# Kernel optimization log

Hardware: AMD Instinct MI355X
Metric: run time of the kernel (lower is better)

The kernel has to match this reference:

```python
import jax, jax.numpy as jnp
import numpy as np

H = 4  # num_heads


def transformer_conv(x, src, dst, wq, bq, wk, bk, wv, bv, ws, bs):
    # PyG TransformerConv, concat=False, root_weight=True, eval mode (no dropout).
    N = x.shape[0]
    C = wq.shape[1] // H  # per-head channels
    q = (x @ wq + bq).reshape(N, H, C)
    k = (x @ wk + bk).reshape(N, H, C)
    v = (x @ wv + bv).reshape(N, H, C)
    # per-edge attention logits: query at dst, key at src
    logits = (q[dst] * k[src]).sum(-1) / jnp.sqrt(jnp.asarray(C, x.dtype))  # [E,H]
    # scatter-softmax over incoming edges of each destination node
    m = jax.lax.stop_gradient(jax.ops.segment_max(logits, dst, num_segments=N))
    m = jnp.where(jnp.isfinite(m), m, jnp.zeros_like(m))
    e = jnp.exp(logits - m[dst])
    denom = jax.ops.segment_sum(e, dst, num_segments=N)
    alpha = e / (denom[dst] + 1e-16)  # [E,H]
    out = jax.ops.segment_sum(alpha[:, :, None] * v[src], dst, num_segments=N)  # [N,H,C]
    return out.mean(axis=1) + x @ ws + bs  # head-average + skip


def setup_inputs() -> dict:
    key = jax.random.key(0)
    ks = jax.random.split(key, 16)
    N, E, D, HID, OUT = 50000, 800000, 128, 32, 40
    s = 0.05
    inp = {
        "x": jax.random.normal(ks[0], (N, D), jnp.float32),
        "edge_index": jax.random.randint(ks[1], (2, E), 0, N, jnp.int64),
        "wq1": jax.random.normal(ks[2], (D, H * HID), jnp.float32) * s,
        "bq1": jnp.zeros((H * HID,), jnp.float32),
        "wk1": jax.random.normal(ks[3], (D, H * HID), jnp.float32) * s,
        "bk1": jnp.zeros((H * HID,), jnp.float32),
        "wv1": jax.random.normal(ks[4], (D, H * HID), jnp.float32) * s,
        "bv1": jnp.zeros((H * HID,), jnp.float32),
        "ws1": jax.random.normal(ks[5], (D, HID), jnp.float32) * s,
        "bs1": jnp.zeros((HID,), jnp.float32),
        "wq2": jax.random.normal(ks[6], (HID, H * HID), jnp.float32) * s,
        "bq2": jnp.zeros((H * HID,), jnp.float32),
        "wk2": jax.random.normal(ks[7], (HID, H * HID), jnp.float32) * s,
        "bk2": jnp.zeros((H * HID,), jnp.float32),
        "wv2": jax.random.normal(ks[8], (HID, H * HID), jnp.float32) * s,
        "bv2": jnp.zeros((H * HID,), jnp.float32),
        "ws2": jax.random.normal(ks[9], (HID, HID), jnp.float32) * s,
        "bs2": jnp.zeros((HID,), jnp.float32),
        "wc": jax.random.normal(ks[10], (HID, OUT), jnp.float32) * s,
        "bc": jnp.zeros((OUT,), jnp.float32),
    }
    return inp


def reference(x, edge_index, wq1, bq1, wk1, bk1, wv1, bv1, ws1, bs1,
              wq2, bq2, wk2, bk2, wv2, bv2, ws2, bs2, wc, bc):
    src, dst = edge_index[0], edge_index[1]
    h = jax.nn.relu(transformer_conv(x, src, dst, wq1, bq1, wk1, bk1, wv1, bv1, ws1, bs1))
    h = jax.nn.relu(transformer_conv(h, src, dst, wq2, bq2, wk2, bk2, wv2, bv2, ws2, bs2))
    return h @ wc + bc
```

## Files before the change

kernel.cpp:

```cpp
#include <hip/hip_runtime.h>
#include <hip/hip_bf16.h>

typedef __attribute__((ext_vector_type(8))) short short8;
typedef __attribute__((ext_vector_type(4))) float floatx4;
typedef __attribute__((ext_vector_type(4))) unsigned short ushort4v;

__device__ inline unsigned short f2bf(float x) {
    unsigned int u = __float_as_uint(x);
    u += 0x7FFFu + ((u >> 16) & 1u);
    return (unsigned short)(u >> 16);
}
__device__ inline float bf2f(unsigned short h) {
    return __uint_as_float(((unsigned int)h) << 16);
}
__device__ inline float blo(unsigned int u) { return __uint_as_float(u << 16); }
__device__ inline float bhi(unsigned int u) { return __uint_as_float(u & 0xFFFF0000u); }

#if defined(__has_builtin)
#if __has_builtin(__builtin_amdgcn_exp2f)
#define EXP2F(x) __builtin_amdgcn_exp2f(x)
#else
#define EXP2F(x) exp2f(x)
#endif
#if __has_builtin(__builtin_amdgcn_update_dpp)
#define HAVE_DPP 1
#endif
#else
#define EXP2F(x) exp2f(x)
#endif

#ifdef HAVE_DPP
template <int CTRL>
__device__ __forceinline__ float dppadd(float x) {
    int s = __builtin_amdgcn_update_dpp(0, __float_as_int(x), CTRL, 0xf, 0xf, true);
    return x + __int_as_float(s);
}
__device__ __forceinline__ float red8(float x) {
    x = dppadd<0xB1>(x);
    x = dppadd<0x4E>(x);
    x = dppadd<0x141>(x);
    return x;
}
__device__ __forceinline__ float xor8add(float x) {
    return dppadd<0x128>(x);
}
#else
__device__ __forceinline__ float red8(float x) {
    x += __shfl_xor(x, 1); x += __shfl_xor(x, 2); x += __shfl_xor(x, 4);
    return x;
}
__device__ __forceinline__ float xor8add(float x) { return x + __shfl_xor(x, 8); }
#endif

template <bool B> struct BC { static constexpr bool value = B; };

__global__ __launch_bounds__(256) void hist_kernel(
    const int* __restrict__ dst, int* __restrict__ deg, int E)
{
    int e = blockIdx.x * blockDim.x + threadIdx.x;
    if (e < E) atomicAdd(&deg[dst[e]], 1);
}

__global__ __launch_bounds__(256) void scan_part(
    const int* __restrict__ deg, int* __restrict__ bsum, int N)
{
    __shared__ int ws[4];
    const int base = blockIdx.x * 1024;
    const int tid = threadIdx.x, lane = tid & 63, w = tid >> 6;
    int s = 0;
#pragma unroll
    for (int j = 0; j < 4; j++) {
        int i = base + j * 256 + tid;
        if (i < N) s += deg[i];
    }
#pragma unroll
    for (int off = 1; off < 64; off <<= 1) s += __shfl_xor(s, off, 64);
    if (lane == 0) ws[w] = s;
    __syncthreads();
    if (tid == 0) bsum[blockIdx.x] = ws[0] + ws[1] + ws[2] + ws[3];
}

__global__ __launch_bounds__(64) void scan_tops(
    const int* __restrict__ bsum, int* __restrict__ boff,
    int* __restrict__ rowptr, int nb, int N)
{
    int lane = threadIdx.x;
    int v = (lane < nb) ? bsum[lane] : 0;
    int inc = v;
#pragma unroll
    for (int off = 1; off < 64; off <<= 1) {
        int t = __shfl_up(inc, off, 64);
        if (lane >= off) inc += t;
    }
    if (lane < nb) boff[lane] = inc - v;
    if (lane == 63) rowptr[N] = inc;
}

__global__ __launch_bounds__(256) void scan_final(
    const int* __restrict__ deg, const int* __restrict__ boff,
    int* __restrict__ rowptr, int* __restrict__ cursor, int N)
{
    __shared__ int woff[4];
    const int base = blockIdx.x * 1024;
    const int tid = threadIdx.x, lane = tid & 63, w = tid >> 6;
    const int i0 = base + tid * 4;
    int v0 = (i0     < N) ? deg[i0]     : 0;
    int v1 = (i0 + 1 < N) ? deg[i0 + 1] : 0;
    int v2 = (i0 + 2 < N) ? deg[i0 + 2] : 0;
    int v3 = (i0 + 3 < N) ? deg[i0 + 3] : 0;
    int ts = v0 + v1 + v2 + v3;
    int inc = ts;
#pragma unroll
    for (int off = 1; off < 64; off <<= 1) {
        int t = __shfl_up(inc, off, 64);
        if (lane >= off) inc += t;
    }
    if (lane == 63) woff[w] = inc;
    __syncthreads();
    int wpre = 0;
    if (w > 0) wpre += woff[0];
    if (w > 1) wpre += woff[1];
    if (w > 2) wpre += woff[2];
    int exc = boff[blockIdx.x] + wpre + inc - ts;
    int p0 = exc, p1 = exc + v0, p2 = p1 + v1, p3 = p2 + v2;
    if (i0     < N) { rowptr[i0]     = p0; cursor[i0]     = p0; }
    if (i0 + 1 < N) { rowptr[i0 + 1] = p1; cursor[i0 + 1] = p1; }
    if (i0 + 2 < N) { rowptr[i0 + 2] = p2; cursor[i0 + 2] = p2; }
    if (i0 + 3 < N) { rowptr[i0 + 3] = p3; cursor[i0 + 3] = p3; }
}

__global__ __launch_bounds__(256) void fill_kernel(
    const int* __restrict__ src, const int* __restrict__ dst,
    int* __restrict__ cursor, int* __restrict__ perm, int E)
{
    int e = blockIdx.x * blockDim.x + threadIdx.x;
    if (e >= E) return;
    int pos = atomicAdd(&cursor[dst[e]], 1);
    perm[pos] = src[e];
}

__global__ __launch_bounds__(128) void wprep_all(
    const float* __restrict__ wq1, const float* __restrict__ bq1,
    const float* __restrict__ wk1, const float* __restrict__ bk1,
    const float* __restrict__ wv1, const float* __restrict__ bv1,
    const float* __restrict__ ws1, const float* __restrict__ bs1,
    const float* __restrict__ wq2, const float* __restrict__ bq2,
    const float* __restrict__ wk2, const float* __restrict__ bk2,
    const float* __restrict__ wv2, const float* __restrict__ bv2,
    const float* __restrict__ ws2, const float* __restrict__ bs2,
    unsigned short* __restrict__ wt1h, unsigned short* __restrict__ wt1l,
    float* __restrict__ bias1,
    unsigned short* __restrict__ wt2h, unsigned short* __restrict__ wt2l,
    float* __restrict__ bias2)
{
    const int layer = (blockIdx.x >= 416) ? 1 : 0;
    const int c = blockIdx.x - layer * 416;
    const int t = threadIdx.x;
    const int L = layer ? 32 : 128;
    if (t >= L) return;
    const float* w; const float* b; int cc, ncols;
    if (c < 384) {
        int m = c >> 7; cc = c & 127; ncols = 128;
        if (layer == 0) {
            w = (m == 0) ? wq1 : ((m == 1) ? wk1 : wv1);
            b = (m == 0) ? bq1 : ((m == 1) ? bk1 : bv1);
        } else {
            w = (m == 0) ? wq2 : ((m == 1) ? wk2 : wv2);
            b = (m == 0) ? bq2 : ((m == 1) ? bk2 : bv2);
        }
    } else {
        cc = c - 384; ncols = 32;
        w = layer ? ws2 : ws1; b = layer ? bs2 : bs1;
    }
    unsigned short* wh = layer ? wt2h : wt1h;
    unsigned short* wl = layer ? wt2l : wt1l;
    float* bias = layer ? bias2 : bias1;
    const float QSCL = 0.17677669529663687f * 1.4426950408889634f;
    const float f = (c < 128) ? QSCL : 1.0f;
    float val = w[t * ncols + cc] * f;
    unsigned short h = f2bf(val);
    wh[c * L + t] = h;
    wl[c * L + t] = f2bf(val - bf2f(h));
    if (t == 0) bias[c] = b[cc] * f;
}

template <int L>
__global__ __launch_bounds__(256) void proj_mfma(
    const float* __restrict__ xin,
    const unsigned short* __restrict__ wt_hi,
    const unsigned short* __restrict__ wt_lo,
    const float* __restrict__ bias,
    float* __restrict__ q, unsigned short* __restrict__ kvp,
    float* __restrict__ skip, int N)
{
    constexpr int LP = L + 8;
    constexpr int KS = L / 32;
    constexpr int SI = (32 * (L / 4)) / 256;
    __shared__ unsigned short xh[2][32 * LP];
    __shared__ unsigned short xl[2][32 * LP];
    __shared__ float scr[4][32 * 36];
    const int tid = threadIdx.x, lane = tid & 63, w = tid >> 6;
    const int li = lane & 15, quad = lane >> 4;
    const int slot = __builtin_amdgcn_readfirstlane(blockIdx.y * 4 + w);
    const bool hasT = slot < 13;

    int t0 = 24, t1 = 25;
    if (slot < 4)       { t0 = slot * 2; t1 = t0 + 1; }
    else if (slot < 12) { t0 = 4 + slot; t1 = 12 + slot; }

    short8 Ah[2][KS], Al[2][KS];
    float bias_r[2][4];
    if (hasT) {
#pragma unroll
        for (int ti = 0; ti < 2; ti++) {
            int tt = ti ? t1 : t0;
#pragma unroll
            for (int ks = 0; ks < KS; ks++) {
                long off = (long)(tt * 16 + li) * L + ks * 32 + quad * 8;
                Ah[ti][ks] = *(const short8*)(wt_hi + off);
                Al[ti][ks] = *(const short8*)(wt_lo + off);
            }
#pragma unroll
            for (int r = 0; r < 4; r++)
                bias_r[ti][r] = bias[tt * 16 + quad * 4 + r];
        }
    }

    const int nb0 = blockIdx.x * 256;
    float* myscr = scr[w];
    unsigned int* su = (unsigned int*)myscr;

    float4 xv[SI];
    auto issue_loads = [&](int c) {
#pragma unroll
        for (int s = 0; s < SI; s++) {
            int f = s * 256 + tid;
            int row = f / (L / 4), c4 = (f - row * (L / 4)) * 4;
            int n = nb0 + c * 32 + row;
            xv[s] = (n < N) ? *(const float4*)(xin + (long)n * L + c4)
                            : make_float4(0.f, 0.f, 0.f, 0.f);
        }
    };
    auto cvt_store = [&](int buf) {
#pragma unroll
        for (int s = 0; s < SI; s++) {
            int f = s * 256 + tid;
            int row = f / (L / 4), c4 = (f - row * (L / 4)) * 4;
            unsigned short h0 = f2bf(xv[s].x), h1 = f2bf(xv[s].y),
                           h2 = f2bf(xv[s].z), h3 = f2bf(xv[s].w);
            ushort4v hs = {h0, h1, h2, h3};
            ushort4v ls = {f2bf(xv[s].x - bf2f(h0)), f2bf(xv[s].y - bf2f(h1)),
                           f2bf(xv[s].z - bf2f(h2)), f2bf(xv[s].w - bf2f(h3))};
            *(ushort4v*)(xh[buf] + row * LP + c4) = hs;
            *(ushort4v*)(xl[buf] + row * LP + c4) = ls;
        }
    };

    issue_loads(0);
    cvt_store(0);
    __syncthreads();

    for (int c = 0; c < 8; c++) {
        if (c < 7) issue_loads(c + 1);
        const int n0c = nb0 + c * 32;
        if (hasT) {
            const int buf = c & 1;
#pragma unroll
            for (int half = 0; half < 2; half++) {
                short8 Bh[KS], Bl[KS];
#pragma unroll
                for (int ks = 0; ks < KS; ks++) {
                    int off = (half * 16 + li) * LP + ks * 32 + quad * 8;
                    Bh[ks] = *(const short8*)(xh[buf] + off);
                    Bl[ks] = *(const short8*)(xl[buf] + off);
                }
                floatx4 accv[2];
#pragma unroll
                for (int ti = 0; ti < 2; ti++) {
                    floatx4 acc = {0.f, 0.f, 0.f, 0.f};
#pragma unroll
                    for (int ks = 0; ks < KS; ks++) {
                        acc = __builtin_amdgcn_mfma_f32_16x16x32_bf16(Ah[ti][ks], Bh[ks], acc, 0, 0, 0);
                        acc = __builtin_amdgcn_mfma_f32_16x16x32_bf16(Ah[ti][ks], Bl[ks], acc, 0, 0, 0);
                        acc = __builtin_amdgcn_mfma_f32_16x16x32_bf16(Al[ti][ks], Bh[ks], acc, 0, 0, 0);
                    }
#pragma unroll
                    for (int r = 0; r < 4; r++) acc[r] += bias_r[ti][r];
                    accv[ti] = acc;
                }
                const int row = half * 16 + li;
                if (slot < 4 || slot == 12) {
                    *(floatx4*)(myscr + row * 36 + quad * 4)      = accv[0];
                    *(floatx4*)(myscr + row * 36 + 16 + quad * 4) = accv[1];
                } else {
                    unsigned int k01 = (unsigned int)f2bf(accv[0][0]) | ((unsigned int)f2bf(accv[0][1]) << 16);
                    unsigned int k23 = (unsigned int)f2bf(accv[0][2]) | ((unsigned int)f2bf(accv[0][3]) << 16);
                    unsigned int v01 = (unsigned int)f2bf(accv[1][0]) | ((unsigned int)f2bf(accv[1][1]) << 16);
                    unsigned int v23 = (unsigned int)f2bf(accv[1][2]) | ((unsigned int)f2bf(accv[1][3]) << 16);
                    uint4 pk = make_uint4(k01, v01, k23, v23);
                    *(uint4*)(su + row * 20 + quad * 4) = pk;
                }
            }
            if (slot < 4) {
#pragma unroll
                for (int it = 0; it < 4; it++) {
                    int idx = it * 64 + lane;
                    int nl = idx >> 3, seg = idx & 7;
                    int node = n0c + nl;
                    if (node < N) {
                        floatx4 vv = *(floatx4*)(myscr + nl * 36 + seg * 4);
                        *(floatx4*)(q + (long)node * 128 + slot * 32 + seg * 4) = vv;
                    }
                }
            } else if (slot == 12) {
#pragma unroll
                for (int it = 0; it < 4; it++) {
                    int idx = it * 64 + lane;
                    int nl = idx >> 3, seg = idx & 7;
                    int node = n0c + nl;
                    if (node < N) {
                        floatx4 vv = *(floatx4*)(myscr + nl * 36 + seg * 4);
                        *(floatx4*)(skip + (long)node * 32 + seg * 4) = vv;
                    }
                }
            } else {
                const int i = slot - 4;
#pragma unroll
                for (int it = 0; it < 2; it++) {
                    int idx = it * 64 + lane;
                    int nl = idx >> 2, part = idx & 3;
                    int node = n0c + nl;
                    if (node < N) {
                        uint4 vv = *(uint4*)(su + nl * 20 + part * 4);
                        *(uint4*)((unsigned int*)(kvp + (long)node * 256) + i * 16 + part * 4) = vv;
                    }
                }
            }
        }
        __syncthreads();
        if (c < 7) cvt_store((c + 1) & 1);
        __syncthreads();
    }
}

template <bool FUSE_CLS>
__global__ __launch_bounds__(256) void attn_kernel(
    const float* __restrict__ q, const unsigned short* __restrict__ kvp,
    const int* __restrict__ rowptr, const int* __restrict__ perm,
    const float* __restrict__ skip, float* __restrict__ h,
    const float* __restrict__ wc, const float* __restrict__ bc,
    float* __restrict__ out, int N, int E)
{
    __shared__ float hrow[4][32];
    const int tid = threadIdx.x;
    const int wid = (blockIdx.x * 256 + tid) >> 6;
    const int wv = (tid >> 6) & 3;
    const int lane = tid & 63;
    if (wid >= N) return;
    const int d = __builtin_amdgcn_readfirstlane(wid);
    const int eh = lane >> 5;
    const int sl = lane & 31;
    const int hh = sl >> 3;
    const int g  = sl & 7;
    const unsigned dby = (unsigned)(hh * 64 + g * 8) * 2u;
    const char* __restrict__ kvb = (const char*)kvp;
    const float4 q4 = *(const float4*)(q + (long)d * 128 + hh * 32 + g * 4);

    const int beg = rowptr[d], end = rowptr[d + 1];
    const int n = end - beg;
    const int na = (n + 1) >> 1;
    const int nmin = n - na;
    const int my_off = beg + (eh ? na : 0);
    const int my_cnt = eh ? nmin : na;
    const int* __restrict__ pp = perm + my_off;

    float den = 0.f;
    float o0 = 0.f, o1 = 0.f, o2 = 0.f, o3 = 0.f;

    auto kvld = [&](int s) -> uint4 {
        return *(const uint4*)(kvb + ((((unsigned)s) << 9) + dby));
    };

    uint4 A0, A1, A2, A3, B0, B1, B2, B3, C0, C1, C2, C3;
    int PA0, PA1, PA2, PA3, PB0, PB1, PB2, PB3, PC0, PC1, PC2, PC3;
    {
        int i0 = pp[0], i1 = pp[1], i2  = pp[2],  i3  = pp[3];
        int i4 = pp[4], i5 = pp[5], i6  = pp[6],  i7  = pp[7];
        int i8 = pp[8], i9 = pp[9], i10 = pp[10], i11 = pp[11];
        PA0 = pp[12]; PA1 = pp[13]; PA2 = pp[14]; PA3 = pp[15];
        PB0 = pp[16]; PB1 = pp[17]; PB2 = pp[18]; PB3 = pp[19];
        PC0 = pp[20]; PC1 = pp[21]; PC2 = pp[22]; PC3 = pp[23];
        A0 = kvld(i0); A1 = kvld(i1); A2 = kvld(i2);  A3 = kvld(i3);
        B0 = kvld(i4); B1 = kvld(i5); B2 = kvld(i6);  B3 = kvld(i7);
        C0 = kvld(i8); C1 = kvld(i9); C2 = kvld(i10); C3 = kvld(i11);
    }

    auto grp = [&](const uint4& G0, const uint4& G1, const uint4& G2,
                   const uint4& G3, int jb, auto mc) {
        constexpr bool MASKED = decltype(mc)::value;
        float p0 = q4.x * blo(G0.x) + q4.y * bhi(G0.x) + q4.z * blo(G0.z) + q4.w * bhi(G0.z);
        float p1 = q4.x * blo(G1.x) + q4.y * bhi(G1.x) + q4.z * blo(G1.z) + q4.w * bhi(G1.z);
        float p2 = q4.x * blo(G2.x) + q4.y * bhi(G2.x) + q4.z * blo(G2.z) + q4.w * bhi(G2.z);
        float p3 = q4.x * blo(G3.x) + q4.y * bhi(G3.x) + q4.z * blo(G3.z) + q4.w * bhi(G3.z);
        p0 = red8(p0); p1 = red8(p1); p2 = red8(p2); p3 = red8(p3);
        p0 = fminf(p0, 60.f); p1 = fminf(p1, 60.f);
        p2 = fminf(p2, 60.f); p3 = fminf(p3, 60.f);
        if (MASKED) {
            p0 = (jb + 0 < my_cnt) ? p0 : -INFINITY;
            p1 = (jb + 1 < my_cnt) ? p1 : -INFINITY;
            p2 = (jb + 2 < my_cnt) ? p2 : -INFINITY;
            p3 = (jb + 3 < my_cnt) ? p3 : -INFINITY;
        }
        const float w0 = EXP2F(p0), w1 = EXP2F(p1);
        const float w2 = EXP2F(p2), w3 = EXP2F(p3);
        den += (w0 + w1) + (w2 + w3);
        o0 += w0 * blo(G0.y) + w1 * blo(G1.y) + w2 * blo(G2.y) + w3 * blo(G3.y);
        o1 += w0 * bhi(G0.y) + w1 * bhi(G1.y) + w2 * bhi(G2.y) + w3 * bhi(G3.y);
        o2 += w0 * blo(G0.w) + w1 * blo(G1.w) + w2 * blo(G2.w) + w3 * blo(G3.w);
        o3 += w0 * bhi(G0.w) + w1 * bhi(G1.w) + w2 * bhi(G2.w) + w3 * bhi(G3.w);
    };

    int j = 0;
    for (; j + 12 <= nmin; j += 12) {
        grp(A0, A1, A2, A3, j, BC<false>{});
        A0 = kvld(PA0); A1 = kvld(PA1); A2 = kvld(PA2); A3 = kvld(PA3);
        PA0 = pp[j + 24]; PA1 = pp[j + 25]; PA2 = pp[j + 26]; PA3 = pp[j + 27];
        grp(B0, B1, B2, B3, j + 4, BC<false>{});
        B0 = kvld(PB0); B1 = kvld(PB1); B2 = kvld(PB2); B3 = kvld(PB3);
        PB0 = pp[j + 28]; PB1 = pp[j + 29]; PB2 = pp[j + 30]; PB3 = pp[j + 31];
        grp(C0, C1, C2, C3, j + 8, BC<false>{});
        C0 = kvld(PC0); C1 = kvld(PC1); C2 = kvld(PC2); C3 = kvld(PC3);
        PC0 = pp[j + 32]; PC1 = pp[j + 33]; PC2 = pp[j + 34]; PC3 = pp[j + 35];
    }
    if (j < na) {
        grp(A0, A1, A2, A3, j, BC<true>{});
        if (j + 4 < na) grp(B0, B1, B2, B3, j + 4, BC<true>{});
        if (j + 8 < na) grp(C0, C1, C2, C3, j + 8, BC<true>{});
    }

    den += __shfl_xor(den, 32);
    o0 += __shfl_xor(o0, 32);
    o1 += __shfl_xor(o1, 32);
    o2 += __shfl_xor(o2, 32);
    o3 += __shfl_xor(o3, 32);

    const float inv = 1.f / (den + 1e-16f);
    o0 *= inv; o1 *= inv; o2 *= inv; o3 *= inv;
    o0 = xor8add(o0); o1 = xor8add(o1);
    o2 = xor8add(o2); o3 = xor8add(o3);
    o0 += __shfl_xor(o0, 16); o1 += __shfl_xor(o1, 16);
    o2 += __shfl_xor(o2, 16); o3 += __shfl_xor(o3, 16);

    if (lane < 8) {
        float4 sk = *(const float4*)(skip + (long)d * 32 + g * 4);
        float r0 = 0.25f * o0 + sk.x;
        float r1 = 0.25f * o1 + sk.y;
        float r2 = 0.25f * o2 + sk.z;
        float r3 = 0.25f * o3 + sk.w;
        r0 = r0 > 0.f ? r0 : 0.f;
        r1 = r1 > 0.f ? r1 : 0.f;
        r2 = r2 > 0.f ? r2 : 0.f;
        r3 = r3 > 0.f ? r3 : 0.f;
        if (FUSE_CLS) {
            *(float4*)&hrow[wv][g * 4] = make_float4(r0, r1, r2, r3);
        } else {
            *(float4*)(h + (long)d * 32 + g * 4) = make_float4(r0, r1, r2, r3);
        }
    }
    if (FUSE_CLS) {
        __builtin_amdgcn_wave_barrier();
        if (lane < 40) {
            float acc = bc[lane];
#pragma unroll
            for (int l = 0; l < 32; ++l)
                acc = fmaf(hrow[wv][l], wc[l * 40 + lane], acc);
            out[(long)d * 40 + lane] = acc;
        }
    }
}

extern "C" void kernel_launch(void* const* d_in, const int* in_sizes, int n_in,
                              void* d_out, int out_size, void* d_ws, size_t ws_size,
                              hipStream_t stream)
{
    const float* x   = (const float*)d_in[0];
    const int* ei    = (const int*)d_in[1];
    const float* wq1 = (const float*)d_in[2];  const float* bq1 = (const float*)d_in[3];
    const float* wk1 = (const float*)d_in[4];  const float* bk1 = (const float*)d_in[5];
    const float* wv1 = (const float*)d_in[6];  const float* bv1 = (const float*)d_in[7];
    const float* ws1 = (const float*)d_in[8];  const float* bs1 = (const float*)d_in[9];
    const float* wq2 = (const float*)d_in[10]; const float* bq2 = (const float*)d_in[11];
    const float* wk2 = (const float*)d_in[12]; const float* bk2 = (const float*)d_in[13];
    const float* wv2 = (const float*)d_in[14]; const float* bv2 = (const float*)d_in[15];
    const float* ws2 = (const float*)d_in[16]; const float* bs2 = (const float*)d_in[17];
    const float* wc  = (const float*)d_in[18]; const float* bc  = (const float*)d_in[19];

    const int N = in_sizes[0] / 128;
    const int E = in_sizes[1] / 2;
    const int* src = ei;
    const int* dst = ei + E;

    char* p = (char*)d_ws;
    auto take = [&](size_t bytes) { char* r = p; p += (bytes + 255) & ~(size_t)255; return r; };
    float* q             = (float*)take((size_t)N * 128 * 4);
    unsigned short* kvp  = (unsigned short*)take((size_t)N * 256 * 2);
    float* skip          = (float*)take((size_t)N * 32 * 4);
    float* h1            = (float*)take((size_t)N * 32 * 4);
    unsigned short* wt1h = (unsigned short*)take(416 * 128 * 2);
    unsigned short* wt1l = (unsigned short*)take(416 * 128 * 2);
    unsigned short* wt2h = (unsigned short*)take(416 * 32 * 2);
    unsigned short* wt2l = (unsigned short*)take(416 * 32 * 2);
    float* bias1         = (float*)take(416 * 4);
    float* bias2         = (float*)take(416 * 4);
    int* deg             = (int*)take((size_t)N * 4);
    int* rowptr          = (int*)take((size_t)(N + 1) * 4);
    int* cursor          = (int*)take((size_t)N * 4);
    int* perm            = (int*)take((size_t)(E + 48) * 4);
    int* bsum            = (int*)take(64 * 4);
    int* boff            = (int*)take(64 * 4);

    const dim3 projGrid((N + 255) / 256, 4);
    const int eGrid    = (E + 255) / 256;
    const int attnGrid = (N + 3) / 4;
    const int nb       = (N + 1023) / 1024;

    wprep_all<<<832, 128, 0, stream>>>(wq1, bq1, wk1, bk1, wv1, bv1, ws1, bs1,
                                       wq2, bq2, wk2, bk2, wv2, bv2, ws2, bs2,
                                       wt1h, wt1l, bias1, wt2h, wt2l, bias2);
    hipMemsetAsync(deg, 0, (size_t)N * 4, stream);
    hipMemsetAsync(perm + E, 0, 48 * 4, stream);
    hist_kernel<<<eGrid, 256, 0, stream>>>(dst, deg, E);
    scan_part<<<nb, 256, 0, stream>>>(deg, bsum, N);
    scan_tops<<<1, 64, 0, stream>>>(bsum, boff, rowptr, nb, N);
    scan_final<<<nb, 256, 0, stream>>>(deg, boff, rowptr, cursor, N);
    fill_kernel<<<eGrid, 256, 0, stream>>>(src, dst, cursor, perm, E);

    proj_mfma<128><<<projGrid, 256, 0, stream>>>(x, wt1h, wt1l, bias1, q, kvp, skip, N);
    attn_kernel<false><<<attnGrid, 256, 0, stream>>>(q, kvp, rowptr, perm, skip, h1,
                                                     wc, bc, (float*)d_out, N, E);

    proj_mfma<32><<<projGrid, 256, 0, stream>>>(h1, wt2h, wt2l, bias2, q, kvp, skip, N);
    attn_kernel<true><<<attnGrid, 256, 0, stream>>>(q, kvp, rowptr, perm, skip, h1,
                                                    wc, bc, (float*)d_out, N, E);
}
```

Baseline: 365.1 us.

## Fuse CSR build kernels into weight prep and projection, load x directly into registers

Merges the weight-prep kernel with the degree histogram, and merges the CSR fill pass into the layer-1 projection launch as extra blocks. The perm padding clear moves into scan_tops, dropping a memset. The projection kernel now runs 512-thread blocks with 8 waves and no LDS staging of x: each wave loads its own x rows from global memory into registers, splits them into bf16 hi/lo, and uses wave barriers instead of block barriers. This removes several launches and the block-wide syncs, at the cost of each wave reloading the same x tile, so global/L2 traffic goes up, and fill atomics now compete with the projection work.

```diff
diff --git a/kernel.cpp b/kernel.cpp
--- a/kernel.cpp
+++ b/kernel.cpp
@@ -3,7 +3,6 @@
 
 typedef __attribute__((ext_vector_type(8))) short short8;
 typedef __attribute__((ext_vector_type(4))) float floatx4;
-typedef __attribute__((ext_vector_type(4))) unsigned short ushort4v;
 
 __device__ inline unsigned short f2bf(float x) {
     unsigned int u = __float_as_uint(x);
@@ -54,11 +53,56 @@
 
 template <bool B> struct BC { static constexpr bool value = B; };
 
-__global__ __launch_bounds__(256) void hist_kernel(
+__global__ __launch_bounds__(256) void wprep_hist(
+    const float* __restrict__ wq1, const float* __restrict__ bq1,
+    const float* __restrict__ wk1, const float* __restrict__ bk1,
+    const float* __restrict__ wv1, const float* __restrict__ bv1,
+    const float* __restrict__ ws1, const float* __restrict__ bs1,
+    const float* __restrict__ wq2, const float* __restrict__ bq2,
+    const float* __restrict__ wk2, const float* __restrict__ bk2,
+    const float* __restrict__ wv2, const float* __restrict__ bv2,
+    const float* __restrict__ ws2, const float* __restrict__ bs2,
+    unsigned short* __restrict__ wt1h, unsigned short* __restrict__ wt1l,
+    float* __restrict__ bias1,
+    unsigned short* __restrict__ wt2h, unsigned short* __restrict__ wt2l,
+    float* __restrict__ bias2,
     const int* __restrict__ dst, int* __restrict__ deg, int E)
 {
-    int e = blockIdx.x * blockDim.x + threadIdx.x;
-    if (e < E) atomicAdd(&deg[dst[e]], 1);
+    const int bx = blockIdx.x;
+    const int t = threadIdx.x;
+    if (bx >= 832) {
+        int e = (bx - 832) * 256 + t;
+        if (e < E) atomicAdd(&deg[dst[e]], 1);
+        return;
+    }
+    const int layer = (bx >= 416) ? 1 : 0;
+    const int c = bx - layer * 416;
+    const int L = layer ? 32 : 128;
+    if (t >= L) return;
+    const float* w; const float* b; int cc, ncols;
+    if (c < 384) {
+        int m = c >> 7; cc = c & 127; ncols = 128;
+        if (layer == 0) {
+            w = (m == 0) ? wq1 : ((m == 1) ? wk1 : wv1);
+            b = (m == 0) ? bq1 : ((m == 1) ? bk1 : bv1);
+        } else {
+            w = (m == 0) ? wq2 : ((m == 1) ? wk2 : wv2);
+            b = (m == 0) ? bq2 : ((m == 1) ? bk2 : bv2);
+        }
+    } else {
+        cc = c - 384; ncols = 32;
+        w = layer ? ws2 : ws1; b = layer ? bs2 : bs1;
+    }
+    unsigned short* wh = layer ? wt2h : wt1h;
+    unsigned short* wl = layer ? wt2l : wt1l;
+    float* bias = layer ? bias2 : bias1;
+    const float QSCL = 0.17677669529663687f * 1.4426950408889634f;
+    const float f = (c < 128) ? QSCL : 1.0f;
+    float val = w[t * ncols + cc] * f;
+    unsigned short h = f2bf(val);
+    wh[c * L + t] = h;
+    wl[c * L + t] = f2bf(val - bf2f(h));
+    if (t == 0) bias[c] = b[cc] * f;
 }
 
 __global__ __launch_bounds__(256) void scan_part(
@@ -82,9 +126,11 @@
 
 __global__ __launch_bounds__(64) void scan_tops(
     const int* __restrict__ bsum, int* __restrict__ boff,
-    int* __restrict__ rowptr, int nb, int N)
+    int* __restrict__ rowptr, int nb, int N,
+    int* __restrict__ perm, int E)
 {
     int lane = threadIdx.x;
+    if (lane < 48) perm[E + lane] = 0;
     int v = (lane < nb) ? bsum[lane] : 0;
     int inc = v;
 #pragma unroll
@@ -129,217 +175,150 @@
     if (i0 + 3 < N) { rowptr[i0 + 3] = p3; cursor[i0 + 3] = p3; }
 }
 
-__global__ __launch_bounds__(256) void fill_kernel(
-    const int* __restrict__ src, const int* __restrict__ dst,
-    int* __restrict__ cursor, int* __restrict__ perm, int E)
-{
-    int e = blockIdx.x * blockDim.x + threadIdx.x;
-    if (e >= E) return;
-    int pos = atomicAdd(&cursor[dst[e]], 1);
-    perm[pos] = src[e];
-}
-
-__global__ __launch_bounds__(128) void wprep_all(
-    const float* __restrict__ wq1, const float* __restrict__ bq1,
-    const float* __restrict__ wk1, const float* __restrict__ bk1,
-    const float* __restrict__ wv1, const float* __restrict__ bv1,
-    const float* __restrict__ ws1, const float* __restrict__ bs1,
-    const float* __restrict__ wq2, const float* __restrict__ bq2,
-    const float* __restrict__ wk2, const float* __restrict__ bk2,
-    const float* __restrict__ wv2, const float* __restrict__ bv2,
-    const float* __restrict__ ws2, const float* __restrict__ bs2,
-    unsigned short* __restrict__ wt1h, unsigned short* __restrict__ wt1l,
-    float* __restrict__ bias1,
-    unsigned short* __restrict__ wt2h, unsigned short* __restrict__ wt2l,
-    float* __restrict__ bias2)
-{
-    const int layer = (blockIdx.x >= 416) ? 1 : 0;
-    const int c = blockIdx.x - layer * 416;
-    const int t = threadIdx.x;
-    const int L = layer ? 32 : 128;
-    if (t >= L) return;
-    const float* w; const float* b; int cc, ncols;
-    if (c < 384) {
-        int m = c >> 7; cc = c & 127; ncols = 128;
-        if (layer == 0) {
-            w = (m == 0) ? wq1 : ((m == 1) ? wk1 : wv1);
-            b = (m == 0) ? bq1 : ((m == 1) ? bk1 : bv1);
-        } else {
-            w = (m == 0) ? wq2 : ((m == 1) ? wk2 : wv2);
-            b = (m == 0) ? bq2 : ((m == 1) ? bk2 : bv2);
-        }
-    } else {
-        cc = c - 384; ncols = 32;
-        w = layer ? ws2 : ws1; b = layer ? bs2 : bs1;
-    }
-    unsigned short* wh = layer ? wt2h : wt1h;
-    unsigned short* wl = layer ? wt2l : wt1l;
-    float* bias = layer ? bias2 : bias1;
-    const float QSCL = 0.17677669529663687f * 1.4426950408889634f;
-    const float f = (c < 128) ? QSCL : 1.0f;
-    float val = w[t * ncols + cc] * f;
-    unsigned short h = f2bf(val);
-    wh[c * L + t] = h;
-    wl[c * L + t] = f2bf(val - bf2f(h));
-    if (t == 0) bias[c] = b[cc] * f;
-}
-
 template <int L>
-__global__ __launch_bounds__(256) void proj_mfma(
+__global__ __launch_bounds__(512) void proj_reg(
     const float* __restrict__ xin,
     const unsigned short* __restrict__ wt_hi,
     const unsigned short* __restrict__ wt_lo,
     const float* __restrict__ bias,
     float* __restrict__ q, unsigned short* __restrict__ kvp,
-    float* __restrict__ skip, int N)
-{
-    constexpr int LP = L + 8;
+    float* __restrict__ skip, int N, int projNB,
+    const int* __restrict__ src, const int* __restrict__ dst,
+    int* __restrict__ cursor, int* __restrict__ perm, int E)
+{
     constexpr int KS = L / 32;
-    constexpr int SI = (32 * (L / 4)) / 256;
-    __shared__ unsigned short xh[2][32 * LP];
-    __shared__ unsigned short xl[2][32 * LP];
-    __shared__ float scr[4][32 * 36];
-    const int tid = threadIdx.x, lane = tid & 63, w = tid >> 6;
+    __shared__ float scr[8][32 * 36];
+
+    const int bx = blockIdx.x;
+    const int tid = threadIdx.x;
+    if (bx >= projNB * 2) {
+        int e = (bx - projNB * 2) * 512 + tid;
+        if (e < E) {
+            int pos = atomicAdd(&cursor[dst[e]], 1);
+            perm[pos] = src[e];
+        }
+        return;
+    }
+
+    const int lane = tid & 63, w = tid >> 6;
     const int li = lane & 15, quad = lane >> 4;
-    const int slot = __builtin_amdgcn_readfirstlane(blockIdx.y * 4 + w);
-    const bool hasT = slot < 13;
-
-    int t0 = 24, t1 = 25;
+    const int slot = __builtin_amdgcn_readfirstlane((bx & 1) * 8 + w);
+    if (slot >= 13) return;
+
+    int t0, t1;
     if (slot < 4)       { t0 = slot * 2; t1 = t0 + 1; }
     else if (slot < 12) { t0 = 4 + slot; t1 = 12 + slot; }
+    else                { t0 = 24; t1 = 25; }
 
     short8 Ah[2][KS], Al[2][KS];
     float bias_r[2][4];
-    if (hasT) {
-#pragma unroll
-        for (int ti = 0; ti < 2; ti++) {
-            int tt = ti ? t1 : t0;
-#pragma unroll
-            for (int ks = 0; ks < KS; ks++) {
-                long off = (long)(tt * 16 + li) * L + ks * 32 + quad * 8;
-                Ah[ti][ks] = *(const short8*)(wt_hi + off);
-                Al[ti][ks] = *(const short8*)(wt_lo + off);
-            }
-#pragma unroll
-            for (int r = 0; r < 4; r++)
-                bias_r[ti][r] = bias[tt * 16 + quad * 4 + r];
-        }
-    }
-
-    const int nb0 = blockIdx.x * 256;
+#pragma unroll
+    for (int ti = 0; ti < 2; ti++) {
+        int tt = ti ? t1 : t0;
+#pragma unroll
+        for (int ks = 0; ks < KS; ks++) {
+            long off = (long)(tt * 16 + li) * L + ks * 32 + quad * 8;
+            Ah[ti][ks] = *(const short8*)(wt_hi + off);
+            Al[ti][ks] = *(const short8*)(wt_lo + off);
+        }
+#pragma unroll
+        for (int r = 0; r < 4; r++)
+            bias_r[ti][r] = bias[tt * 16 + quad * 4 + r];
+    }
+
+    const int nb0 = (bx >> 1) * 256;
     float* myscr = scr[w];
     unsigned int* su = (unsigned int*)myscr;
 
-    float4 xv[SI];
-    auto issue_loads = [&](int c) {
-#pragma unroll
-        for (int s = 0; s < SI; s++) {
-            int f = s * 256 + tid;
-            int row = f / (L / 4), c4 = (f - row * (L / 4)) * 4;
-            int n = nb0 + c * 32 + row;
-            xv[s] = (n < N) ? *(const float4*)(xin + (long)n * L + c4)
-                            : make_float4(0.f, 0.f, 0.f, 0.f);
-        }
-    };
-    auto cvt_store = [&](int buf) {
-#pragma unroll
-        for (int s = 0; s < SI; s++) {
-            int f = s * 256 + tid;
-            int row = f / (L / 4), c4 = (f - row * (L / 4)) * 4;
-            unsigned short h0 = f2bf(xv[s].x), h1 = f2bf(xv[s].y),
-                           h2 = f2bf(xv[s].z), h3 = f2bf(xv[s].w);
-            ushort4v hs = {h0, h1, h2, h3};
-            ushort4v ls = {f2bf(xv[s].x - bf2f(h0)), f2bf(xv[s].y - bf2f(h1)),
-                           f2bf(xv[s].z - bf2f(h2)), f2bf(xv[s].w - bf2f(h3))};
-            *(ushort4v*)(xh[buf] + row * LP + c4) = hs;
-            *(ushort4v*)(xl[buf] + row * LP + c4) = ls;
-        }
-    };
-
-    issue_loads(0);
-    cvt_store(0);
-    __syncthreads();
-
     for (int c = 0; c < 8; c++) {
-        if (c < 7) issue_loads(c + 1);
         const int n0c = nb0 + c * 32;
-        if (hasT) {
-            const int buf = c & 1;
-#pragma unroll
-            for (int half = 0; half < 2; half++) {
-                short8 Bh[KS], Bl[KS];
+#pragma unroll
+        for (int half = 0; half < 2; half++) {
+            const int node = n0c + half * 16 + li;
+            const bool ok = node < N;
+            const float* xr = xin + (long)node * L;
+            short8 Bh[KS], Bl[KS];
+#pragma unroll
+            for (int ks = 0; ks < KS; ks++) {
+                float4 f0 = ok ? *(const float4*)(xr + ks * 32 + quad * 8)
+                               : make_float4(0.f, 0.f, 0.f, 0.f);
+                float4 f1 = ok ? *(const float4*)(xr + ks * 32 + quad * 8 + 4)
+                               : make_float4(0.f, 0.f, 0.f, 0.f);
+                unsigned short h0 = f2bf(f0.x), h1 = f2bf(f0.y),
+                               h2 = f2bf(f0.z), h3 = f2bf(f0.w);
+                unsigned short h4 = f2bf(f1.x), h5 = f2bf(f1.y),
+                               h6 = f2bf(f1.z), h7 = f2bf(f1.w);
+                Bh[ks] = (short8){(short)h0, (short)h1, (short)h2, (short)h3,
+                                  (short)h4, (short)h5, (short)h6, (short)h7};
+                Bl[ks] = (short8){(short)f2bf(f0.x - bf2f(h0)), (short)f2bf(f0.y - bf2f(h1)),
+                                  (short)f2bf(f0.z - bf2f(h2)), (short)f2bf(f0.w - bf2f(h3)),
+                                  (short)f2bf(f1.x - bf2f(h4)), (short)f2bf(f1.y - bf2f(h5)),
+                                  (short)f2bf(f1.z - bf2f(h6)), (short)f2bf(f1.w - bf2f(h7))};
+            }
+            floatx4 accv[2];
+#pragma unroll
+            for (int ti = 0; ti < 2; ti++) {
+                floatx4 acc = {0.f, 0.f, 0.f, 0.f};
 #pragma unroll
                 for (int ks = 0; ks < KS; ks++) {
-                    int off = (half * 16 + li) * LP + ks * 32 + quad * 8;
-                    Bh[ks] = *(const short8*)(xh[buf] + off);
-                    Bl[ks] = *(const short8*)(xl[buf] + off);
+                    acc = __builtin_amdgcn_mfma_f32_16x16x32_bf16(Ah[ti][ks], Bh[ks], acc, 0, 0, 0);
+                    acc = __builtin_amdgcn_mfma_f32_16x16x32_bf16(Ah[ti][ks], Bl[ks], acc, 0, 0, 0);
+                    acc = __builtin_amdgcn_mfma_f32_16x16x32_bf16(Al[ti][ks], Bh[ks], acc, 0, 0, 0);
                 }
-                floatx4 accv[2];
-#pragma unroll
-                for (int ti = 0; ti < 2; ti++) {
-                    floatx4 acc = {0.f, 0.f, 0.f, 0.f};
-#pragma unroll
-                    for (int ks = 0; ks < KS; ks++) {
-                        acc = __builtin_amdgcn_mfma_f32_16x16x32_bf16(Ah[ti][ks], Bh[ks], acc, 0, 0, 0);
-                        acc = __builtin_amdgcn_mfma_f32_16x16x32_bf16(Ah[ti][ks], Bl[ks], acc, 0, 0, 0);
-                        acc = __builtin_amdgcn_mfma_f32_16x16x32_bf16(Al[ti][ks], Bh[ks], acc, 0, 0, 0);
-                    }
-#pragma unroll
-                    for (int r = 0; r < 4; r++) acc[r] += bias_r[ti][r];
-                    accv[ti] = acc;
-                }
-                const int row = half * 16 + li;
-                if (slot < 4 || slot == 12) {
-                    *(floatx4*)(myscr + row * 36 + quad * 4)      = accv[0];
-                    *(floatx4*)(myscr + row * 36 + 16 + quad * 4) = accv[1];
-                } else {
-                    unsigned int k01 = (unsigned int)f2bf(accv[0][0]) | ((unsigned int)f2bf(accv[0][1]) << 16);
-                    unsigned int k23 = (unsigned int)f2bf(accv[0][2]) | ((unsigned int)f2bf(accv[0][3]) << 16);
-                    unsigned int v01 = (unsigned int)f2bf(accv[1][0]) | ((unsigned int)f2bf(accv[1][1]) << 16);
-                    unsigned int v23 = (unsigned int)f2bf(accv[1][2]) | ((unsigned int)f2bf(accv[1][3]) << 16);
-                    uint4 pk = make_uint4(k01, v01, k23, v23);
-                    *(uint4*)(su + row * 20 + quad * 4) = pk;
+#pragma unroll
+                for (int r = 0; r < 4; r++) acc[r] += bias_r[ti][r];
+                accv[ti] = acc;
+            }
+            const int row = half * 16 + li;
+            if (slot < 4 || slot == 12) {
+                *(floatx4*)(myscr + row * 36 + quad * 4)      = accv[0];
+                *(floatx4*)(myscr + row * 36 + 16 + quad * 4) = accv[1];
+            } else {
+                unsigned int k01 = (unsigned int)f2bf(accv[0][0]) | ((unsigned int)f2bf(accv[0][1]) << 16);
+                unsigned int k23 = (unsigned int)f2bf(accv[0][2]) | ((unsigned int)f2bf(accv[0][3]) << 16);
+                unsigned int v01 = (unsigned int)f2bf(accv[1][0]) | ((unsigned int)f2bf(accv[1][1]) << 16);
+                unsigned int v23 = (unsigned int)f2bf(accv[1][2]) | ((unsigned int)f2bf(accv[1][3]) << 16);
+                uint4 pk = make_uint4(k01, v01, k23, v23);
+                *(uint4*)(su + row * 20 + quad * 4) = pk;
+            }
+        }
+        __builtin_amdgcn_wave_barrier();
+        if (slot < 4) {
+#pragma unroll
+            for (int it = 0; it < 4; it++) {
+                int idx = it * 64 + lane;
+                int nl = idx >> 3, seg = idx & 7;
+                int node = n0c + nl;
+                if (node < N) {
+                    floatx4 vv = *(floatx4*)(myscr + nl * 36 + seg * 4);
+                    *(floatx4*)(q + (long)node * 128 + slot * 32 + seg * 4) = vv;
                 }
             }
-            if (slot < 4) {
-#pragma unroll
-                for (int it = 0; it < 4; it++) {
-                    int idx = it * 64 + lane;
-                    int nl = idx >> 3, seg = idx & 7;
-                    int node = n0c + nl;
-                    if (node < N) {
-                        floatx4 vv = *(floatx4*)(myscr + nl * 36 + seg * 4);
-                        *(floatx4*)(q + (long)node * 128 + slot * 32 + seg * 4) = vv;
-                    }
-                }
-            } else if (slot == 12) {
-#pragma unroll
-                for (int it = 0; it < 4; it++) {
-                    int idx = it * 64 + lane;
-                    int nl = idx >> 3, seg = idx & 7;
-                    int node = n0c + nl;
-                    if (node < N) {
-                        floatx4 vv = *(floatx4*)(myscr + nl * 36 + seg * 4);
-                        *(floatx4*)(skip + (long)node * 32 + seg * 4) = vv;
-                    }
-                }
-            } else {
-                const int i = slot - 4;
-#pragma unroll
-                for (int it = 0; it < 2; it++) {
-                    int idx = it * 64 + lane;
-                    int nl = idx >> 2, part = idx & 3;
-                    int node = n0c + nl;
-                    if (node < N) {
-                        uint4 vv = *(uint4*)(su + nl * 20 + part * 4);
-                        *(uint4*)((unsigned int*)(kvp + (long)node * 256) + i * 16 + part * 4) = vv;
-                    }
+        } else if (slot == 12) {
+#pragma unroll
+            for (int it = 0; it < 4; it++) {
+                int idx = it * 64 + lane;
+                int nl = idx >> 3, seg = idx & 7;
+                int node = n0c + nl;
+                if (node < N) {
+                    floatx4 vv = *(floatx4*)(myscr + nl * 36 + seg * 4);
+                    *(floatx4*)(skip + (long)node * 32 + seg * 4) = vv;
                 }
             }
-        }
-        __syncthreads();
-        if (c < 7) cvt_store((c + 1) & 1);
-        __syncthreads();
+        } else {
+            const int i = slot - 4;
+#pragma unroll
+            for (int it = 0; it < 2; it++) {
+                int idx = it * 64 + lane;
+                int nl = idx >> 2, part = idx & 3;
+                int node = n0c + nl;
+                if (node < N) {
+                    uint4 vv = *(uint4*)(su + nl * 20 + part * 4);
+                    *(uint4*)((unsigned int*)(kvp + (long)node * 256) + i * 16 + part * 4) = vv;
+                }
+            }
+        }
+        __builtin_amdgcn_wave_barrier();
     }
 }
 
@@ -519,27 +498,31 @@
     int* bsum            = (int*)take(64 * 4);
     int* boff            = (int*)take(64 * 4);
 
-    const dim3 projGrid((N + 255) / 256, 4);
-    const int eGrid    = (E + 255) / 256;
+    const int projNB   = (N + 255) / 256;
+    const int eGrid256 = (E + 255) / 256;
+    const int eGrid512 = (E + 511) / 512;
     const int attnGrid = (N + 3) / 4;
     const int nb       = (N + 1023) / 1024;
 
-    wprep_all<<<832, 128, 0, stream>>>(wq1, bq1, wk1, bk1, wv1, bv1, ws1, bs1,
-                                       wq2, bq2, wk2, bk2, wv2, bv2, ws2, bs2,
-                                       wt1h, wt1l, bias1, wt2h, wt2l, bias2);
     hipMemsetAsync(deg, 0, (size_t)N * 4, stream);
-    hipMemsetAsync(perm + E, 0, 48 * 4, stream);
-    hist_kernel<<<eGrid, 256, 0, stream>>>(dst, deg, E);
+    wprep_hist<<<832 + eGrid256, 256, 0, stream>>>(
+        wq1, bq1, wk1, bk1, wv1, bv1, ws1, bs1,
+        wq2, bq2, wk2, bk2, wv2, bv2, ws2, bs2,
+        wt1h, wt1l, bias1, wt2h, wt2l, bias2,
+        dst, deg, E);
     scan_part<<<nb, 256, 0, stream>>>(deg, bsum, N);
-    scan_tops<<<1, 64, 0, stream>>>(bsum, boff, rowptr, nb, N);
+    scan_tops<<<1, 64, 0, stream>>>(bsum, boff, rowptr, nb, N, perm, E);
     scan_final<<<nb, 256, 0, stream>>>(deg, boff, rowptr, cursor, N);
-    fill_kernel<<<eGrid, 256, 0, stream>>>(src, dst, cursor, perm, E);
-
-    proj_mfma<128><<<projGrid, 256, 0, stream>>>(x, wt1h, wt1l, bias1, q, kvp, skip, N);
+
+    proj_reg<128><<<projNB * 2 + eGrid512, 512, 0, stream>>>(
+        x, wt1h, wt1l, bias1, q, kvp, skip, N, projNB,
+        src, dst, cursor, perm, E);
     attn_kernel<false><<<attnGrid, 256, 0, stream>>>(q, kvp, rowptr, perm, skip, h1,
                                                      wc, bc, (float*)d_out, N, E);
 
-    proj_mfma<32><<<projGrid, 256, 0, stream>>>(h1, wt2h, wt2l, bias2, q, kvp, skip, N);
+    proj_reg<32><<<projNB * 2, 512, 0, stream>>>(
+        h1, wt2h, wt2l, bias2, q, kvp, skip, N, projNB,
+        src, dst, cursor, perm, 0);
     attn_kernel<true><<<attnGrid, 256, 0, stream>>>(q, kvp, rowptr, perm, skip, h1,
                                                     wc, bc, (float*)d_out, N, E);
 }
```

Result: no change. 364.5 us (-0.1%).
